# Optimization experiments

Measured on AMD Instinct MI355X. Metric: run time of the kernel, lower is better.

Reference implementation:

```python
import jax, jax.numpy as jnp
import numpy as np

B, S, HID = 2, 2048, 2048
NH, NKV, D = 16, 4, 128
EPS = 1e-6
THETA = 1000000.0
SCALE = D ** -0.5


def _rmsnorm(x, w):
    # per-head RMSNorm over last dim (head_dim)
    var = jnp.mean(x * x, axis=-1, keepdims=True)
    return x * jax.lax.rsqrt(var + EPS) * w


def _rope(pos, x):
    # neox-style rotary over full head_dim. x: [B,S,h,D], pos: [B,S]
    half = D // 2
    inv_freq = THETA ** (-jnp.arange(half, dtype=jnp.float32) / half)  # theta^(-2i/D)
    freqs = pos.astype(jnp.float32)[..., None] * inv_freq              # [B,S,half]
    cos = jnp.cos(freqs)[:, :, None, :]
    sin = jnp.sin(freqs)[:, :, None, :]
    x1, x2 = x[..., :half], x[..., half:]
    return jnp.concatenate([x1 * cos - x2 * sin, x2 * cos + x1 * sin], axis=-1)


def setup_inputs() -> dict:
    key = jax.random.key(0)
    ks = jax.random.split(key, 6)
    hidden_states = jax.random.normal(ks[0], (B, S, HID), dtype=jnp.float32)
    positions = jnp.tile(jnp.arange(S, dtype=jnp.int32)[None, :], (B, 1))
    sd = 0.02
    Wq = jax.random.normal(ks[1], (HID, NH * D), dtype=jnp.float32) * sd
    Wk = jax.random.normal(ks[2], (HID, NKV * D), dtype=jnp.float32) * sd
    Wv = jax.random.normal(ks[3], (HID, NKV * D), dtype=jnp.float32) * sd
    Wo = jax.random.normal(ks[4], (NH * D, HID), dtype=jnp.float32) * sd
    q_norm_w = jnp.ones((D,), dtype=jnp.float32)
    k_norm_w = jnp.ones((D,), dtype=jnp.float32)
    return {"hidden_states": hidden_states, "positions": positions,
            "Wq": Wq, "Wk": Wk, "Wv": Wv, "Wo": Wo,
            "q_norm_w": q_norm_w, "k_norm_w": k_norm_w}


def reference(hidden_states, positions, Wq, Wk, Wv, Wo, q_norm_w, k_norm_w):
    # QKV projections (no bias)
    q = (hidden_states @ Wq).reshape(B, S, NH, D)
    k = (hidden_states @ Wk).reshape(B, S, NKV, D)
    v = (hidden_states @ Wv).reshape(B, S, NKV, D)
    # per-head RMSNorm
    q = _rmsnorm(q, q_norm_w)
    k = _rmsnorm(k, k_norm_w)
    # rotary embedding
    q = _rope(positions, q)
    k = _rope(positions, k)
    # GQA: expand kv heads to q heads
    rep = NH // NKV
    k = jnp.repeat(k, rep, axis=2)  # [B,S,NH,D]
    v = jnp.repeat(v, rep, axis=2)
    # non-causal (ENCODER_ONLY) attention
    scores = jnp.einsum('bqhd,bkhd->bhqk', q, k) * SCALE
    attn = jax.nn.softmax(scores, axis=-1)
    ctx = jnp.einsum('bhqk,bkhd->bqhd', attn, v).reshape(B, S, NH * D)
    out = ctx @ Wo
    return out
```

## Files before the change

kernel.cpp:

```cpp
#include <hip/hip_runtime.h>

typedef unsigned short ushort_t;
typedef __attribute__((ext_vector_type(8))) short short8;
typedef __attribute__((ext_vector_type(4))) float f32x4;

#define Bb 2
#define Ss 2048
#define HID 2048
#define NH 16
#define NKV 4
#define Dd 128
constexpr float EPS_ = 1e-6f;
constexpr float THETA_ = 1000000.0f;
constexpr float SCALE_ = 0.08838834764831845f;
constexpr float C2_ = 0.12753785f;

__device__ __forceinline__ ushort_t f2bf(float x) {
  union { float f; unsigned u; } v; v.f = x;
  unsigned r = (v.u + 0x7fffu + ((v.u >> 16) & 1u)) >> 16;
  return (ushort_t)r;
}
__device__ __forceinline__ float bf2f(ushort_t u) {
  union { unsigned u; float f; } v; v.u = ((unsigned)u) << 16;
  return v.f;
}

typedef const __attribute__((address_space(1))) void* gas1_t;
typedef __attribute__((address_space(3))) void* las3_t;
__device__ __forceinline__ void gload_lds16(const void* g, void* l) {
  __builtin_amdgcn_global_load_lds((gas1_t)g, (las3_t)l, 16, 0, 0);
}

__device__ __forceinline__ void store_out(float* p, float v) { *p = v; }
__device__ __forceinline__ void store_out(ushort_t* p, float v) { *p = f2bf(v); }

__global__ __launch_bounds__(256) void convert_f32_bf16(
    const float* __restrict__ src, ushort_t* __restrict__ dst, long n) {
  long i = ((long)blockIdx.x * 256 + threadIdx.x) * 4;
  if (i + 3 < n) {
    float4 v = *(const float4*)(src + i);
    ushort_t o0 = f2bf(v.x), o1 = f2bf(v.y), o2 = f2bf(v.z), o3 = f2bf(v.w);
    ushort_t* d = dst + i;
    d[0] = o0; d[1] = o1; d[2] = o2; d[3] = o3;
  }
}

__global__ __launch_bounds__(256) void transpose_f32_bf16(
    const float* __restrict__ src, ushort_t* __restrict__ dst, int R, int C) {
  __shared__ float tile[32][33];
  int c0 = blockIdx.x * 32, r0 = blockIdx.y * 32;
  int tx = threadIdx.x & 31, ty = threadIdx.x >> 5;
#pragma unroll
  for (int j = 0; j < 4; j++)
    tile[ty + j * 8][tx] = src[(long)(r0 + ty + j * 8) * C + c0 + tx];
  __syncthreads();
#pragma unroll
  for (int j = 0; j < 4; j++)
    dst[(long)(c0 + ty + j * 8) * R + r0 + tx] = f2bf(tile[tx][ty + j * 8]);
}

template <typename OutT>
__global__ __launch_bounds__(256) void gemm_bt(
    const ushort_t* __restrict__ A, const ushort_t* __restrict__ Bt,
    OutT* __restrict__ C, int M, int N, int K) {
  __shared__ __align__(16) ushort_t As[128 * 32];
  __shared__ __align__(16) ushort_t Bs[128 * 32];
  const int t = threadIdx.x;
  const int wave = t >> 6, lane = t & 63;
  const int wr = wave >> 1, wc = wave & 1;
  const int quad = lane >> 4, l16 = lane & 15;
  const long bm = (long)blockIdx.y * 128, bn = (long)blockIdx.x * 128;

  f32x4 acc[4][4] = {};

  const int srow = t >> 2, schunk = t & 3;
  const ushort_t* aSrc = A + (bm + srow) * (long)K + schunk * 8;
  const ushort_t* bSrc = Bt + (bn + srow) * (long)K + schunk * 8;
  const int ldsOff = srow * 32 + schunk * 8;

  for (int k0 = 0; k0 < K; k0 += 32) {
    __syncthreads();
    gload_lds16(aSrc + k0, &As[ldsOff]);
    gload_lds16(aSrc + (long)64 * K + k0, &As[ldsOff + 64 * 32]);
    gload_lds16(bSrc + k0, &Bs[ldsOff]);
    gload_lds16(bSrc + (long)64 * K + k0, &Bs[ldsOff + 64 * 32]);
    __syncthreads();
    short8 af[4], bf[4];
#pragma unroll
    for (int i = 0; i < 4; i++) {
      af[i] = *(const short8*)&As[(wr * 64 + i * 16 + l16) * 32 + quad * 8];
      bf[i] = *(const short8*)&Bs[(wc * 64 + i * 16 + l16) * 32 + quad * 8];
    }
#pragma unroll
    for (int i = 0; i < 4; i++)
#pragma unroll
      for (int j = 0; j < 4; j++)
        acc[i][j] = __builtin_amdgcn_mfma_f32_16x16x32_bf16(af[i], bf[j], acc[i][j], 0, 0, 0);
  }
#pragma unroll
  for (int i = 0; i < 4; i++)
#pragma unroll
    for (int j = 0; j < 4; j++)
#pragma unroll
      for (int r = 0; r < 4; r++) {
        long rr = bm + wr * 64 + i * 16 + quad * 4 + r;
        long cc = bn + wc * 64 + j * 16 + l16;
        store_out(&C[rr * N + cc], acc[i][j][r]);
      }
}

__global__ __launch_bounds__(256) void rmsnorm_rope(
    ushort_t* __restrict__ qkv, const int* __restrict__ positions,
    const float* __restrict__ qw, const float* __restrict__ kw) {
  int gw = blockIdx.x * 4 + (threadIdx.x >> 6);
  int lane = threadIdx.x & 63;
  int bs = gw / 20, h = gw % 20;
  ushort_t* src = qkv + (long)bs * 3072 + h * 128;
  float x0 = bf2f(src[lane]), x1 = bf2f(src[lane + 64]);
  float ss = x0 * x0 + x1 * x1;
#pragma unroll
  for (int off = 32; off; off >>= 1) ss += __shfl_xor(ss, off);
  float r = rsqrtf(ss * (1.0f / 128.0f) + EPS_);
  const float* w = (h < 16) ? qw : kw;
  x0 = x0 * r * w[lane];
  x1 = x1 * r * w[lane + 64];
  float pos = (float)positions[bs];
  float inv_freq = powf(THETA_, -(float)lane * (1.0f / 64.0f));
  float f = pos * inv_freq;
  float sn, cs;
  sincosf(f, &sn, &cs);
  float o0 = x0 * cs - x1 * sn;
  float o1 = x1 * cs + x0 * sn;
  src[lane] = f2bf(o0);
  src[lane + 64] = f2bf(o1);
}

__global__ __launch_bounds__(256) void transpose_v(
    const ushort_t* __restrict__ qkv, ushort_t* __restrict__ Vt) {
  __shared__ ushort_t tile[64][65];
  int bh = blockIdx.z;
  int s0 = blockIdx.x * 64, d0 = blockIdx.y * 64;
  int b = bh >> 2, hk = bh & 3;
  int tx = threadIdx.x & 63, ty = threadIdx.x >> 6;
#pragma unroll
  for (int j = 0; j < 16; j++) {
    int sl = j * 4 + ty;
    tile[sl][tx] = qkv[(long)(b * Ss + s0 + sl) * 3072 + 2560 + hk * 128 + d0 + tx];
  }
  __syncthreads();
  const long vtbase = (long)bh * Dd * Ss;
#pragma unroll
  for (int j = 0; j < 16; j++) {
    int dl = j * 4 + ty;
    Vt[vtbase + (long)(d0 + dl) * Ss + s0 + tx] = tile[tx][dl];
  }
}

__global__ __launch_bounds__(256, 4) void flash_attn(
    const ushort_t* __restrict__ qkv, const ushort_t* __restrict__ Vt,
    ushort_t* __restrict__ ctx) {
  __shared__ __align__(16) ushort_t Ks[64 * 128];
  __shared__ __align__(16) ushort_t Vs[128 * 64];
  __shared__ __align__(16) ushort_t Ps[4][16 * 64];
  const int qt = blockIdx.x, h = blockIdx.y, b = blockIdx.z;
  const int hk = h >> 2;
  const int t = threadIdx.x, wave = t >> 6, lane = t & 63;
  const int quad = lane >> 4, l16 = lane & 15;

  const ushort_t* qp = qkv + (long)(b * Ss + qt * 64) * 3072 + h * 128;
  const ushort_t* kp = qkv + (long)(b * Ss) * 3072 + 2048 + hk * 128;
  const ushort_t* vp = Vt + ((long)(b * NKV + hk) * Dd) * Ss;

  short8 qf[4];
  {
    const ushort_t* qrow = qp + (long)(wave * 16 + l16) * 3072 + quad * 8;
#pragma unroll
    for (int kc = 0; kc < 4; kc++)
      qf[kc] = *(const short8*)(qrow + kc * 32);
  }

  float m_i[4] = {-1e30f, -1e30f, -1e30f, -1e30f};
  float l_i[4] = {0.f, 0.f, 0.f, 0.f};
  f32x4 o[8] = {};

  for (int kt = 0; kt < Ss / 64; kt++) {
    const int k0 = kt * 64;
    __syncthreads();
#pragma unroll
    for (int it = 0; it < 4; it++) {
      int tt = t + it * 256;
      int row = tt >> 4, cl = tt & 15, cg = cl ^ (row & 15);
      gload_lds16(kp + (long)(k0 + row) * 3072 + cg * 8, &Ks[tt * 8]);
    }
#pragma unroll
    for (int it = 0; it < 4; it++) {
      int tt = t + it * 256;
      int row = tt >> 3, cl = tt & 7, cg = cl ^ (row & 7);
      gload_lds16(vp + (long)row * Ss + k0 + cg * 8, &Vs[tt * 8]);
    }
    __syncthreads();

    f32x4 sa[4] = {};
#pragma unroll
    for (int kc = 0; kc < 4; kc++) {
#pragma unroll
      for (int nt = 0; nt < 4; nt++) {
        int brow = nt * 16 + l16;
        short8 bfr = *(const short8*)&Ks[brow * 128 + (((kc * 4 + quad) ^ (brow & 15)) * 8)];
        sa[nt] = __builtin_amdgcn_mfma_f32_16x16x32_bf16(qf[kc], bfr, sa[nt], 0, 0, 0);
      }
    }

    float mc[4], alpha[4];
#pragma unroll
    for (int r = 0; r < 4; r++) {
      float mx = fmaxf(fmaxf(sa[0][r], sa[1][r]), fmaxf(sa[2][r], sa[3][r]));
#pragma unroll
      for (int off = 8; off; off >>= 1) mx = fmaxf(mx, __shfl_xor(mx, off));
      float mnew = fmaxf(m_i[r], mx);
      alpha[r] = __builtin_amdgcn_exp2f((m_i[r] - mnew) * C2_);
      m_i[r] = mnew;
      mc[r] = mnew * C2_;
    }
    float rs[4] = {0.f, 0.f, 0.f, 0.f};
#pragma unroll
    for (int nt = 0; nt < 4; nt++)
#pragma unroll
      for (int r = 0; r < 4; r++) {
        float p = __builtin_amdgcn_exp2f(__builtin_fmaf(sa[nt][r], C2_, -mc[r]));
        sa[nt][r] = p;
        rs[r] += p;
      }
#pragma unroll
    for (int r = 0; r < 4; r++) {
#pragma unroll
      for (int off = 8; off; off >>= 1) rs[r] += __shfl_xor(rs[r], off);
      l_i[r] = l_i[r] * alpha[r] + rs[r];
    }
#pragma unroll
    for (int nt = 0; nt < 4; nt++)
#pragma unroll
      for (int r = 0; r < 4; r++) {
        int row = quad * 4 + r, col = nt * 16 + l16;
        int cg = col >> 3, ci = col & 7;
        int cl = cg ^ (row & 7);
        union { float f; unsigned u; } pv; pv.f = sa[nt][r];
        Ps[wave][row * 64 + cl * 8 + ci] = (ushort_t)((pv.u + 0x8000u) >> 16);
      }
    asm volatile("s_waitcnt lgkmcnt(0)" ::: "memory");
#pragma unroll
    for (int dt = 0; dt < 8; dt++)
#pragma unroll
      for (int r = 0; r < 4; r++) o[dt][r] *= alpha[r];
#pragma unroll
    for (int kc = 0; kc < 2; kc++) {
      int arow = l16;
      short8 af = *(const short8*)&Ps[wave][arow * 64 + (((kc * 4 + quad) ^ (arow & 7)) * 8)];
#pragma unroll
      for (int dt = 0; dt < 8; dt++) {
        int brow = dt * 16 + l16;
        short8 bfr = *(const short8*)&Vs[brow * 64 + (((kc * 4 + quad) ^ (brow & 7)) * 8)];
        o[dt] = __builtin_amdgcn_mfma_f32_16x16x32_bf16(af, bfr, o[dt], 0, 0, 0);
      }
    }
  }
  const long obase = (long)(b * Ss + qt * 64 + wave * 16) * (NH * Dd) + h * Dd;
#pragma unroll
  for (int dt = 0; dt < 8; dt++)
#pragma unroll
    for (int r = 0; r < 4; r++) {
      int row = quad * 4 + r, col = dt * 16 + l16;
      ctx[obase + (long)row * (NH * Dd) + col] = f2bf(o[dt][r] / l_i[r]);
    }
}

extern "C" void kernel_launch(void* const* d_in, const int* in_sizes, int n_in,
                              void* d_out, int out_size, void* d_ws, size_t ws_size,
                              hipStream_t stream) {
  const float* hidden = (const float*)d_in[0];
  const int* positions = (const int*)d_in[1];
  const float* Wq = (const float*)d_in[2];
  const float* Wk = (const float*)d_in[3];
  const float* Wv = (const float*)d_in[4];
  const float* Wo = (const float*)d_in[5];
  const float* qw = (const float*)d_in[6];
  const float* kw = (const float*)d_in[7];
  float* out = (float*)d_out;

  char* ws = (char*)d_ws;
  ushort_t* Xbf = (ushort_t*)(ws);
  ushort_t* WqkvT = (ushort_t*)(ws + (16l << 20));
  ushort_t* WoT = (ushort_t*)(ws + (28l << 20));
  ushort_t* qkvb = (ushort_t*)(ws + (36l << 20));
  ushort_t* Vt = (ushort_t*)(ws + (60l << 20));
  ushort_t* ctx = Xbf;

  const long nX = (long)Bb * Ss * HID;
  convert_f32_bf16<<<(unsigned)(nX / 4 / 256), 256, 0, stream>>>(hidden, Xbf, nX);
  transpose_f32_bf16<<<dim3(2048 / 32, 2048 / 32), 256, 0, stream>>>(Wq, WqkvT, 2048, 2048);
  transpose_f32_bf16<<<dim3(512 / 32, 2048 / 32), 256, 0, stream>>>(Wk, WqkvT + (long)2048 * 2048, 2048, 512);
  transpose_f32_bf16<<<dim3(512 / 32, 2048 / 32), 256, 0, stream>>>(Wv, WqkvT + (long)2560 * 2048, 2048, 512);
  transpose_f32_bf16<<<dim3(2048 / 32, 2048 / 32), 256, 0, stream>>>(Wo, WoT, 2048, 2048);

  gemm_bt<ushort_t><<<dim3(3072 / 128, 4096 / 128), 256, 0, stream>>>(Xbf, WqkvT, qkvb, 4096, 3072, 2048);

  rmsnorm_rope<<<(Bb * Ss * 20) / 4, 256, 0, stream>>>(qkvb, positions, qw, kw);
  transpose_v<<<dim3(Ss / 64, Dd / 64, Bb * NKV), 256, 0, stream>>>(qkvb, Vt);

  flash_attn<<<dim3(Ss / 64, NH, Bb), 256, 0, stream>>>(qkvb, Vt, ctx);

  gemm_bt<float><<<dim3(2048 / 128, 4096 / 128), 256, 0, stream>>>(ctx, WoT, out, 4096, 2048, 2048);
}
```

Before: 418.3 us.

## Prefetch next K/V tile into registers to overlap loads with compute

Replaces the direct global-to-LDS loads of the K and V tiles with register-staged loads. The next tile is issued into registers right after the current tile is written to shared memory, so its global latency overlaps with the QK^T, softmax and PV work. Address computation is hoisted out of the loop, and the output rescale by alpha is moved before the LDS wait. This costs 32 extra VGPRs per thread for staging, which may lower occupancy, and the last iteration reloads a redundant tile.

```diff
diff --git a/kernel.cpp b/kernel.cpp
--- a/kernel.cpp
+++ b/kernel.cpp
@@ -179,24 +179,46 @@
       qf[kc] = *(const short8*)(qrow + kc * 32);
   }
 
+  const ushort_t* kga[4];
+  const ushort_t* vga[4];
+  int ldsoff[4];
+#pragma unroll
+  for (int it = 0; it < 4; it++) {
+    int tt = t + it * 256;
+    int rowk = tt >> 4, cgk = (tt & 15) ^ (rowk & 15);
+    kga[it] = kp + (long)rowk * 3072 + cgk * 8;
+    int rowv = tt >> 3, cgv = (tt & 7) ^ (rowv & 7);
+    vga[it] = vp + (long)rowv * Ss + cgv * 8;
+    ldsoff[it] = tt * 8;
+  }
+
+  int4 kreg[4], vreg[4];
+#pragma unroll
+  for (int it = 0; it < 4; it++) {
+    kreg[it] = *(const int4*)(kga[it]);
+    vreg[it] = *(const int4*)(vga[it]);
+  }
+
   float m_i[4] = {-1e30f, -1e30f, -1e30f, -1e30f};
   float l_i[4] = {0.f, 0.f, 0.f, 0.f};
   f32x4 o[8] = {};
 
   for (int kt = 0; kt < Ss / 64; kt++) {
-    const int k0 = kt * 64;
     __syncthreads();
 #pragma unroll
     for (int it = 0; it < 4; it++) {
-      int tt = t + it * 256;
-      int row = tt >> 4, cl = tt & 15, cg = cl ^ (row & 15);
-      gload_lds16(kp + (long)(k0 + row) * 3072 + cg * 8, &Ks[tt * 8]);
-    }
-#pragma unroll
-    for (int it = 0; it < 4; it++) {
-      int tt = t + it * 256;
-      int row = tt >> 3, cl = tt & 7, cg = cl ^ (row & 7);
-      gload_lds16(vp + (long)row * Ss + k0 + cg * 8, &Vs[tt * 8]);
+      *(int4*)&Ks[ldsoff[it]] = kreg[it];
+      *(int4*)&Vs[ldsoff[it]] = vreg[it];
+    }
+    {
+      const int ktn = (kt < Ss / 64 - 1) ? kt + 1 : kt;
+      const long koff = (long)ktn * 64 * 3072;
+      const int voff = ktn * 64;
+#pragma unroll
+      for (int it = 0; it < 4; it++) {
+        kreg[it] = *(const int4*)(kga[it] + koff);
+        vreg[it] = *(const int4*)(vga[it] + voff);
+      }
     }
     __syncthreads();
 
@@ -247,11 +269,11 @@
         union { float f; unsigned u; } pv; pv.f = sa[nt][r];
         Ps[wave][row * 64 + cl * 8 + ci] = (ushort_t)((pv.u + 0x8000u) >> 16);
       }
+#pragma unroll
+    for (int dt = 0; dt < 8; dt++)
+#pragma unroll
+      for (int r = 0; r < 4; r++) o[dt][r] *= alpha[r];
     asm volatile("s_waitcnt lgkmcnt(0)" ::: "memory");
-#pragma unroll
-    for (int dt = 0; dt < 8; dt++)
-#pragma unroll
-      for (int r = 0; r < 4; r++) o[dt][r] *= alpha[r];
 #pragma unroll
     for (int kc = 0; kc < 2; kc++) {
       int arow = l16;
```

After: 666.4 us. 59.3% more time.

## Process two 16-row query tiles per wave in flash attention

Applied to the files above, without the earlier changes.

Each wave now handles 32 query rows instead of 16, so a block covers 128 queries and each K/V tile loaded into shared memory is reused across twice as many rows. This halves the grid and the total K/V global traffic, and each B-fragment read from LDS now feeds two MFMAs. In exchange, register pressure roughly doubles for accumulators and Q fragments, so the launch bound drops to 2 waves per SIMD, and with fewer blocks (512) occupancy is lower.

```diff
diff --git a/kernel.cpp b/kernel.cpp
--- a/kernel.cpp
+++ b/kernel.cpp
@@ -156,32 +156,33 @@
   }
 }
 
-__global__ __launch_bounds__(256, 4) void flash_attn(
+__global__ __launch_bounds__(256, 2) void flash_attn(
     const ushort_t* __restrict__ qkv, const ushort_t* __restrict__ Vt,
     ushort_t* __restrict__ ctx) {
   __shared__ __align__(16) ushort_t Ks[64 * 128];
   __shared__ __align__(16) ushort_t Vs[128 * 64];
-  __shared__ __align__(16) ushort_t Ps[4][16 * 64];
+  __shared__ __align__(16) ushort_t Ps[4][32 * 64];
   const int qt = blockIdx.x, h = blockIdx.y, b = blockIdx.z;
   const int hk = h >> 2;
   const int t = threadIdx.x, wave = t >> 6, lane = t & 63;
   const int quad = lane >> 4, l16 = lane & 15;
 
-  const ushort_t* qp = qkv + (long)(b * Ss + qt * 64) * 3072 + h * 128;
+  const ushort_t* qp = qkv + (long)(b * Ss + qt * 128) * 3072 + h * 128;
   const ushort_t* kp = qkv + (long)(b * Ss) * 3072 + 2048 + hk * 128;
   const ushort_t* vp = Vt + ((long)(b * NKV + hk) * Dd) * Ss;
 
-  short8 qf[4];
-  {
-    const ushort_t* qrow = qp + (long)(wave * 16 + l16) * 3072 + quad * 8;
+  short8 qf[2][4];
+#pragma unroll
+  for (int mt = 0; mt < 2; mt++) {
+    const ushort_t* qrow = qp + (long)(wave * 32 + mt * 16 + l16) * 3072 + quad * 8;
 #pragma unroll
     for (int kc = 0; kc < 4; kc++)
-      qf[kc] = *(const short8*)(qrow + kc * 32);
-  }
-
-  float m_i[4] = {-1e30f, -1e30f, -1e30f, -1e30f};
-  float l_i[4] = {0.f, 0.f, 0.f, 0.f};
-  f32x4 o[8] = {};
+      qf[mt][kc] = *(const short8*)(qrow + kc * 32);
+  }
+
+  float m_i[2][4] = {{-1e30f, -1e30f, -1e30f, -1e30f}, {-1e30f, -1e30f, -1e30f, -1e30f}};
+  float l_i[2][4] = {};
+  f32x4 o[2][8] = {};
 
   for (int kt = 0; kt < Ss / 64; kt++) {
     const int k0 = kt * 64;
@@ -200,78 +201,95 @@
     }
     __syncthreads();
 
-    f32x4 sa[4] = {};
+    f32x4 sa[2][4] = {};
 #pragma unroll
     for (int kc = 0; kc < 4; kc++) {
 #pragma unroll
       for (int nt = 0; nt < 4; nt++) {
         int brow = nt * 16 + l16;
         short8 bfr = *(const short8*)&Ks[brow * 128 + (((kc * 4 + quad) ^ (brow & 15)) * 8)];
-        sa[nt] = __builtin_amdgcn_mfma_f32_16x16x32_bf16(qf[kc], bfr, sa[nt], 0, 0, 0);
-      }
-    }
-
-    float mc[4], alpha[4];
-#pragma unroll
-    for (int r = 0; r < 4; r++) {
-      float mx = fmaxf(fmaxf(sa[0][r], sa[1][r]), fmaxf(sa[2][r], sa[3][r]));
-#pragma unroll
-      for (int off = 8; off; off >>= 1) mx = fmaxf(mx, __shfl_xor(mx, off));
-      float mnew = fmaxf(m_i[r], mx);
-      alpha[r] = __builtin_amdgcn_exp2f((m_i[r] - mnew) * C2_);
-      m_i[r] = mnew;
-      mc[r] = mnew * C2_;
-    }
-    float rs[4] = {0.f, 0.f, 0.f, 0.f};
-#pragma unroll
-    for (int nt = 0; nt < 4; nt++)
+#pragma unroll
+        for (int mt = 0; mt < 2; mt++)
+          sa[mt][nt] = __builtin_amdgcn_mfma_f32_16x16x32_bf16(qf[mt][kc], bfr, sa[mt][nt], 0, 0, 0);
+      }
+    }
+
+    float alpha[2][4];
+#pragma unroll
+    for (int mt = 0; mt < 2; mt++) {
+      float mc[4];
 #pragma unroll
       for (int r = 0; r < 4; r++) {
-        float p = __builtin_amdgcn_exp2f(__builtin_fmaf(sa[nt][r], C2_, -mc[r]));
-        sa[nt][r] = p;
-        rs[r] += p;
-      }
-#pragma unroll
-    for (int r = 0; r < 4; r++) {
-#pragma unroll
-      for (int off = 8; off; off >>= 1) rs[r] += __shfl_xor(rs[r], off);
-      l_i[r] = l_i[r] * alpha[r] + rs[r];
-    }
-#pragma unroll
-    for (int nt = 0; nt < 4; nt++)
+        float mx = fmaxf(fmaxf(sa[mt][0][r], sa[mt][1][r]), fmaxf(sa[mt][2][r], sa[mt][3][r]));
+#pragma unroll
+        for (int off = 8; off; off >>= 1) mx = fmaxf(mx, __shfl_xor(mx, off));
+        float mnew = fmaxf(m_i[mt][r], mx);
+        alpha[mt][r] = __builtin_amdgcn_exp2f((m_i[mt][r] - mnew) * C2_);
+        m_i[mt][r] = mnew;
+        mc[r] = mnew * C2_;
+      }
+      float rs[4] = {0.f, 0.f, 0.f, 0.f};
+#pragma unroll
+      for (int nt = 0; nt < 4; nt++)
+#pragma unroll
+        for (int r = 0; r < 4; r++) {
+          float p = __builtin_amdgcn_exp2f(__builtin_fmaf(sa[mt][nt][r], C2_, -mc[r]));
+          sa[mt][nt][r] = p;
+          rs[r] += p;
+        }
 #pragma unroll
       for (int r = 0; r < 4; r++) {
-        int row = quad * 4 + r, col = nt * 16 + l16;
-        int cg = col >> 3, ci = col & 7;
-        int cl = cg ^ (row & 7);
-        union { float f; unsigned u; } pv; pv.f = sa[nt][r];
-        Ps[wave][row * 64 + cl * 8 + ci] = (ushort_t)((pv.u + 0x8000u) >> 16);
-      }
+#pragma unroll
+        for (int off = 8; off; off >>= 1) rs[r] += __shfl_xor(rs[r], off);
+        l_i[mt][r] = l_i[mt][r] * alpha[mt][r] + rs[r];
+      }
+#pragma unroll
+      for (int nt = 0; nt < 4; nt++)
+#pragma unroll
+        for (int r = 0; r < 4; r++) {
+          int row = mt * 16 + quad * 4 + r, col = nt * 16 + l16;
+          int cg = col >> 3, ci = col & 7;
+          int cl = cg ^ (row & 7);
+          union { float f; unsigned u; } pv; pv.f = sa[mt][nt][r];
+          Ps[wave][row * 64 + cl * 8 + ci] = (ushort_t)((pv.u + 0x8000u) >> 16);
+        }
+    }
+#pragma unroll
+    for (int mt = 0; mt < 2; mt++)
+#pragma unroll
+      for (int dt = 0; dt < 8; dt++)
+#pragma unroll
+        for (int r = 0; r < 4; r++) o[mt][dt][r] *= alpha[mt][r];
     asm volatile("s_waitcnt lgkmcnt(0)" ::: "memory");
 #pragma unroll
-    for (int dt = 0; dt < 8; dt++)
-#pragma unroll
-      for (int r = 0; r < 4; r++) o[dt][r] *= alpha[r];
-#pragma unroll
     for (int kc = 0; kc < 2; kc++) {
-      int arow = l16;
-      short8 af = *(const short8*)&Ps[wave][arow * 64 + (((kc * 4 + quad) ^ (arow & 7)) * 8)];
+      short8 af[2];
+#pragma unroll
+      for (int mt = 0; mt < 2; mt++) {
+        int arow = mt * 16 + l16;
+        af[mt] = *(const short8*)&Ps[wave][arow * 64 + (((kc * 4 + quad) ^ (arow & 7)) * 8)];
+      }
 #pragma unroll
       for (int dt = 0; dt < 8; dt++) {
         int brow = dt * 16 + l16;
         short8 bfr = *(const short8*)&Vs[brow * 64 + (((kc * 4 + quad) ^ (brow & 7)) * 8)];
-        o[dt] = __builtin_amdgcn_mfma_f32_16x16x32_bf16(af, bfr, o[dt], 0, 0, 0);
-      }
-    }
-  }
-  const long obase = (long)(b * Ss + qt * 64 + wave * 16) * (NH * Dd) + h * Dd;
-#pragma unroll
-  for (int dt = 0; dt < 8; dt++)
-#pragma unroll
-    for (int r = 0; r < 4; r++) {
-      int row = quad * 4 + r, col = dt * 16 + l16;
-      ctx[obase + (long)row * (NH * Dd) + col] = f2bf(o[dt][r] / l_i[r]);
-    }
+#pragma unroll
+        for (int mt = 0; mt < 2; mt++)
+          o[mt][dt] = __builtin_amdgcn_mfma_f32_16x16x32_bf16(af[mt], bfr, o[mt][dt], 0, 0, 0);
+      }
+    }
+  }
+#pragma unroll
+  for (int mt = 0; mt < 2; mt++) {
+    const long obase = (long)(b * Ss + qt * 128 + wave * 32 + mt * 16) * (NH * Dd) + h * Dd;
+#pragma unroll
+    for (int dt = 0; dt < 8; dt++)
+#pragma unroll
+      for (int r = 0; r < 4; r++) {
+        int row = quad * 4 + r, col = dt * 16 + l16;
+        ctx[obase + (long)row * (NH * Dd) + col] = f2bf(o[mt][dt][r] / l_i[mt][r]);
+      }
+  }
 }
 
 extern "C" void kernel_launch(void* const* d_in, const int* in_sizes, int n_in,
@@ -307,7 +325,7 @@
   rmsnorm_rope<<<(Bb * Ss * 20) / 4, 256, 0, stream>>>(qkvb, positions, qw, kw);
   transpose_v<<<dim3(Ss / 64, Dd / 64, Bb * NKV), 256, 0, stream>>>(qkvb, Vt);
 
-  flash_attn<<<dim3(Ss / 64, NH, Bb), 256, 0, stream>>>(qkvb, Vt, ctx);
+  flash_attn<<<dim3(Ss / 128, NH, Bb), 256, 0, stream>>>(qkvb, Vt, ctx);
 
   gemm_bt<float><<<dim3(2048 / 128, 4096 / 128), 256, 0, stream>>>(ctx, WoT, out, 4096, 2048, 2048);
 }
```

Result: faster. 401.9 us (-3.9%).
